# Kernel optimization log

Measured on AMD Instinct MI355X. Metric: run time of the kernel, lower is better.

Reference implementation:

```python
import jax, jax.numpy as jnp
import numpy as np

N, E, F, H = 50000, 800000, 128, 8
D = F // H
SCALING = D ** (-0.5)


def setup_inputs() -> dict:
    key = jax.random.key(0)
    ks = jax.random.split(key, 10)
    w_scale = (2.0 / (F + F)) ** 0.5  # approx xavier
    return {
        "feat": jax.random.normal(ks[0], (N, F), jnp.float32),
        "edge_feat": jax.random.normal(ks[1], (E, F), jnp.float32),
        "Wq": jax.random.normal(ks[2], (F, F), jnp.float32) * w_scale,
        "Wk": jax.random.normal(ks[3], (F, F), jnp.float32) * w_scale,
        "Wv": jax.random.normal(ks[4], (F, F), jnp.float32) * w_scale,
        "Wnode": jax.random.normal(ks[5], (F, F), jnp.float32) * w_scale,
        "Wedge": jax.random.normal(ks[6], (H, F), jnp.float32) * w_scale,
        "Wgate": jax.random.normal(ks[7], (H, F), jnp.float32) * w_scale,
        "src": jax.random.randint(ks[8], (E,), 0, N, jnp.int32),
        "dst": jax.random.randint(ks[9], (E,), 0, N, jnp.int32),
    }


def reference(feat, edge_feat, Wq, Wk, Wv, Wnode, Wedge, Wgate, src, dst):
    # dense projections: [N, F] -> [N, H, D]
    q = (feat @ Wq.T).reshape(N, H, D)
    k = (feat @ Wk.T).reshape(N, H, D)
    v = (feat @ Wv.T).reshape(N, H, D)

    # u_dot_v: per-edge, per-head dot product q[src] . k[dst]  -> [E, H]
    a = jnp.einsum("ehd,ehd->eh", q[src], k[dst])

    # edge bias and sigmoid gates from edge features (use_efeats=True)
    e_bias = edge_feat @ Wedge.T            # [E, H]
    gates = jax.nn.sigmoid(edge_feat @ Wgate.T)  # [E, H]

    # clamp, add bias, divide by scaling (i.e. multiply by sqrt(D), as in source)
    logits = (jnp.clip(a, -5.0, 5.0) + e_bias) / SCALING  # [E, H]

    # edge softmax: segmented (per-destination-node) softmax over incoming edges
    m = jax.ops.segment_max(logits, dst, num_segments=N)  # [N, H]
    ex = jnp.exp(logits - m[dst])                          # [E, H]
    s = jax.ops.segment_sum(ex, dst, num_segments=N)       # [N, H]
    sa = (ex / s[dst]) * gates                             # [E, H]

    # weighted scatter-aggregation: sum_e v[src_e] * sa_e grouped by dst
    agg = jax.ops.segment_sum(v[src] * sa[:, :, None], dst, num_segments=N)  # [N, H, D]

    rst = agg.reshape(N, F) @ Wnode.T  # [N, F]
    return rst
```

## Files before the change

kernel.cpp:

```cpp
#include <hip/hip_runtime.h>
#include <hip/hip_fp16.h>
#include <math.h>

#define NN 50000
#define NE 800000
#define FF 128
#define QKV_BLOCKS 782
#define EDGE_GEMM_BLOCKS 12500
#define AGG_BLOCKS 12500
#define HIST_BLOCKS 3125

using short8 = __attribute__((ext_vector_type(8))) short;
using f32x4  = __attribute__((ext_vector_type(4))) float;
using h2     = __attribute__((ext_vector_type(2))) _Float16;

#define EXP_SCALE 5.770780163555851f

__device__ __forceinline__ short f2bf(float x){
  union { float f; unsigned u; } c; c.f = x;
  unsigned r = c.u + 0x7FFFu + ((c.u >> 16) & 1u);
  return (short)(r >> 16);
}
__device__ __forceinline__ float bf2f(short h){
  union { unsigned u; float f; } c; c.u = ((unsigned)(unsigned short)h) << 16;
  return c.f;
}
__device__ __forceinline__ float hdot2(h2 a, h2 b){
#if __has_builtin(__builtin_amdgcn_fdot2)
  return __builtin_amdgcn_fdot2(a, b, 0.f, false);
#else
  return (float)a[0]*(float)b[0] + (float)a[1]*(float)b[1];
#endif
}
__device__ __forceinline__ float fexp2(float x){
#if __has_builtin(__builtin_amdgcn_exp2f)
  return __builtin_amdgcn_exp2f(x);
#else
  return exp2f(x);
#endif
}
__device__ __forceinline__ float clamp5(float x){
#if __has_builtin(__builtin_amdgcn_fmed3f)
  return __builtin_amdgcn_fmed3f(x, -5.f, 5.f);
#else
  return fminf(fmaxf(x, -5.f), 5.f);
#endif
}

#define PREP_A_FRAGS(arow)                                              \
  short8 ahi[4], alo[4];                                                \
  {                                                                     \
    _Pragma("unroll")                                                   \
    for (int kk = 0; kk < 4; kk++){                                     \
      float4 lo4 = *(const float4*)((arow) + kk*32);                    \
      float4 hi4 = *(const float4*)((arow) + kk*32 + 4);                \
      float xs[8] = {lo4.x, lo4.y, lo4.z, lo4.w, hi4.x, hi4.y, hi4.z, hi4.w}; \
      short8 th, tl;                                                    \
      _Pragma("unroll")                                                 \
      for (int j = 0; j < 8; j++){                                      \
        short hh = f2bf(xs[j]);                                         \
        th[j] = hh;                                                     \
        tl[j] = f2bf(xs[j] - bf2f(hh));                                 \
      }                                                                 \
      ahi[kk] = th; alo[kk] = tl;                                       \
    }                                                                   \
  }

#define GEMM_CT_3CHAIN(bh, bl, accout)                                  \
  f32x4 accout;                                                         \
  {                                                                     \
    f32x4 a1 = {0.f,0.f,0.f,0.f}, a2 = {0.f,0.f,0.f,0.f}, a3 = {0.f,0.f,0.f,0.f}; \
    _Pragma("unroll")                                                   \
    for (int kk = 0; kk < 4; kk++){                                     \
      short8 bfh = *(const short8*)((bh) + kk*32);                      \
      short8 bfl = *(const short8*)((bl) + kk*32);                      \
      a1 = __builtin_amdgcn_mfma_f32_16x16x32_bf16(ahi[kk], bfh, a1, 0, 0, 0); \
      a2 = __builtin_amdgcn_mfma_f32_16x16x32_bf16(ahi[kk], bfl, a2, 0, 0, 0); \
      a3 = __builtin_amdgcn_mfma_f32_16x16x32_bf16(alo[kk], bfh, a3, 0, 0, 0); \
    }                                                                   \
    accout = a1 + a2 + a3;                                              \
  }

__global__ void k_cvt_w(const float* __restrict__ Wq, const float* __restrict__ Wk,
                        const float* __restrict__ Wv, const float* __restrict__ Wn,
                        const float* __restrict__ We, const float* __restrict__ Wg,
                        short* bqkv, short* bn, short* bc, int* __restrict__ deg){
  int i = blockIdx.x*256 + threadIdx.x;
  if (i < NN) deg[i] = 0;
  if (i < 16384){
    const float* W[3] = {Wq, Wk, Wv};
    #pragma unroll
    for (int j = 0; j < 3; j++){
      float x = W[j][i];
      short hi = f2bf(x);
      bqkv[j*16384 + i] = hi;
      bqkv[49152 + j*16384 + i] = f2bf(x - bf2f(hi));
    }
    float xn = Wn[i];
    short hn = f2bf(xn);
    bn[i] = hn; bn[i + 16384] = f2bf(xn - bf2f(hn));
  }
  if (i < 2048){
    float x = (i < 1024) ? We[i] : Wg[i-1024];
    short hi = f2bf(x);
    bc[i] = hi; bc[i + 2048] = f2bf(x - bf2f(hi));
  }
}

__global__ void k_qkv_hist(const float* __restrict__ A, const short* __restrict__ B,
                           _Float16* __restrict__ C,
                           const int* __restrict__ dst, int* __restrict__ deg){
  if (blockIdx.x >= QKV_BLOCKS){
    int e = (blockIdx.x - QKV_BLOCKS)*256 + threadIdx.x;
    if (e < NE) atomicAdd(&deg[dst[e]], 1);
    return;
  }
  const int NC = 384;
  int w = threadIdx.x >> 6, lane = threadIdx.x & 63;
  int row0 = (blockIdx.x*4 + w)*16;
  if (row0 >= NN) return;
  int r  = lane & 15;
  int kq = lane >> 4;

  const short* Bhi = B;
  const short* Blo = B + (size_t)NC*FF;

  const float* arow = A + (size_t)(row0 + r)*FF + kq*8;
  PREP_A_FRAGS(arow)

  for (int ct = 0; ct < (NC >> 4); ct++){
    const short* bh = Bhi + (size_t)(ct*16 + r)*FF + kq*8;
    const short* bl = Blo + (size_t)(ct*16 + r)*FF + kq*8;
    GEMM_CT_3CHAIN(bh, bl, acc)
    _Float16* crow = C + (size_t)(row0 + kq*4)*NC + ct*16 + r;
    #pragma unroll
    for (int i = 0; i < 4; i++) crow[(size_t)i*NC] = (_Float16)acc[i];
  }
}

__global__ void k_scan(const int* __restrict__ deg, int* __restrict__ rowptr,
                       int* __restrict__ cursor){
  __shared__ int sums[1024];
  const int CH = 52;
  int t = threadIdx.x;
  int base = t*CH;
  int vals[CH];
  int s = 0;
  #pragma unroll
  for (int i = 0; i < 13; i++){
    int idx = base + i*4;
    int4 v;
    if (idx + 3 < NN) v = *(const int4*)(deg + idx);
    else v = make_int4(idx < NN ? deg[idx] : 0, idx+1 < NN ? deg[idx+1] : 0,
                       idx+2 < NN ? deg[idx+2] : 0, idx+3 < NN ? deg[idx+3] : 0);
    vals[i*4+0]=v.x; vals[i*4+1]=v.y; vals[i*4+2]=v.z; vals[i*4+3]=v.w;
    s += v.x + v.y + v.z + v.w;
  }
  sums[t] = s; __syncthreads();
  for (int off = 1; off < 1024; off <<= 1){
    int val = (t >= off) ? sums[t-off] : 0;
    __syncthreads();
    sums[t] += val;
    __syncthreads();
  }
  int run = sums[t] - s;
  #pragma unroll
  for (int i = 0; i < 13; i++){
    int idx = base + i*4;
    int4 w0;
    w0.x = run; run += vals[i*4+0];
    w0.y = run; run += vals[i*4+1];
    w0.z = run; run += vals[i*4+2];
    w0.w = run; run += vals[i*4+3];
    if (idx + 3 < NN){
      *(int4*)(rowptr + idx) = w0;
      *(int4*)(cursor + idx) = w0;
    } else {
      if (idx   < NN){ rowptr[idx  ] = w0.x; cursor[idx  ] = w0.x; }
      if (idx+1 < NN){ rowptr[idx+1] = w0.y; cursor[idx+1] = w0.y; }
      if (idx+2 < NN){ rowptr[idx+2] = w0.z; cursor[idx+2] = w0.z; }
      if (idx+3 < NN){ rowptr[idx+3] = w0.w; cursor[idx+3] = w0.w; }
    }
  }
}

__global__ void k_edge(const float* __restrict__ A, const short* __restrict__ B,
                       const int* __restrict__ src, const int* __restrict__ dst,
                       int* __restrict__ cursor, int2* __restrict__ list,
                       float* __restrict__ ebg2){
  int w = threadIdx.x >> 6, lane = threadIdx.x & 63;
  int row0 = (blockIdx.x*4 + w)*16;
  int r  = lane & 15;
  int kq = lane >> 4;

  if (kq == 0){
    int e = row0 + r;
    int d = dst[e];
    int s = src[e];
    int pos = atomicAdd(&cursor[d], 1);
    list[pos] = make_int2(s, e);
  }

  const float* arow = A + (size_t)(row0 + r)*FF + kq*8;
  PREP_A_FRAGS(arow)

  const short* bh = B + (size_t)r*FF + kq*8;
  const short* bl = bh + 2048;
  GEMM_CT_3CHAIN(bh, bl, acc)

  #pragma unroll
  for (int i = 0; i < 4; i++){
    int e = row0 + kq*4 + i;
    float x = acc[i];
    float outv; int col;
    if (r < 8){ outv = x*EXP_SCALE; col = r*2; }
    else      { outv = 1.f/(1.f + __expf(-x)); col = (r-8)*2 + 1; }
    ebg2[(size_t)e*16 + col] = outv;
  }
}

__global__ void k_aggregate(const _Float16* __restrict__ qkv, const float* __restrict__ ebg2,
                            const int* __restrict__ rowptr, const int* __restrict__ cursor,
                            const int2* __restrict__ list, float* __restrict__ agg){
  int w = threadIdx.x >> 6, lane = threadIdx.x & 63;
  int node = blockIdx.x*4 + w;
  if (node >= NN) return;
  int beg = rowptr[node], end = cursor[node];
  h2 kk = *(const h2*)&qkv[(size_t)node*384 + 128 + lane*2];
  int h = lane >> 3;
  float ssA=0.f, a0A=0.f, a1A=0.f;
  float ssB=0.f, a0B=0.f, a1B=0.f;
  for (int i0 = beg; i0 < end; i0 += 64){
    int nb = min(end - i0, 64);
    int2 es = (i0 + lane < end) ? list[i0 + lane] : make_int2(0,0);
    int j = 0;
    for (; j + 1 < nb; j += 2){
      int sA = __shfl(es.x, j);
      int eA = __shfl(es.y, j);
      int sB = __shfl(es.x, j+1);
      int eB = __shfl(es.y, j+1);
      const _Float16* rA = qkv + (size_t)sA*384 + lane*2;
      const _Float16* rB = qkv + (size_t)sB*384 + lane*2;
      h2 qA = *(const h2*)rA;
      h2 vA = *(const h2*)(rA + 256);
      h2 qB = *(const h2*)rB;
      h2 vB = *(const h2*)(rB + 256);
      float2 ebA = *(const float2*)&ebg2[(size_t)eA*16 + h*2];
      float2 ebB = *(const float2*)&ebg2[(size_t)eB*16 + h*2];
      float pA = hdot2(qA, kk);
      float pB = hdot2(qB, kk);
      pA += __shfl_xor(pA, 1); pB += __shfl_xor(pB, 1);
      pA += __shfl_xor(pA, 2); pB += __shfl_xor(pB, 2);
      pA += __shfl_xor(pA, 4); pB += __shfl_xor(pB, 4);
      float tA = fexp2(fmaf(clamp5(pA), EXP_SCALE, ebA.x));
      float tB = fexp2(fmaf(clamp5(pB), EXP_SCALE, ebB.x));
      float wA = tA * ebA.y;
      float wB = tB * ebB.y;
      a0A += wA*(float)vA[0]; a1A += wA*(float)vA[1]; ssA += tA;
      a0B += wB*(float)vB[0]; a1B += wB*(float)vB[1]; ssB += tB;
    }
    if (j < nb){
      int sA = __shfl(es.x, j);
      int eA = __shfl(es.y, j);
      const _Float16* rA = qkv + (size_t)sA*384 + lane*2;
      h2 qA = *(const h2*)rA;
      h2 vA = *(const h2*)(rA + 256);
      float2 ebA = *(const float2*)&ebg2[(size_t)eA*16 + h*2];
      float pA = hdot2(qA, kk);
      pA += __shfl_xor(pA, 1); pA += __shfl_xor(pA, 2); pA += __shfl_xor(pA, 4);
      float tA = fexp2(fmaf(clamp5(pA), EXP_SCALE, ebA.x));
      float wA = tA * ebA.y;
      a0A += wA*(float)vA[0]; a1A += wA*(float)vA[1]; ssA += tA;
    }
  }
  float ss = ssA + ssB;
  float inv = (end > beg) ? 1.f/ss : 0.f;
  *(float2*)&agg[(size_t)node*FF + lane*2] = make_float2((a0A+a0B)*inv, (a1A+a1B)*inv);
}

__global__ void k_gemm_out(const float* __restrict__ A, const short* __restrict__ B,
                           float* __restrict__ C){
  const int NC = 128;
  int w = threadIdx.x >> 6, lane = threadIdx.x & 63;
  int row0 = (blockIdx.x*4 + w)*16;
  if (row0 >= NN) return;
  int r  = lane & 15;
  int kq = lane >> 4;

  const short* Bhi = B;
  const short* Blo = B + (size_t)NC*FF;

  const float* arow = A + (size_t)(row0 + r)*FF + kq*8;
  PREP_A_FRAGS(arow)

  for (int ct = 0; ct < (NC >> 4); ct++){
    const short* bh = Bhi + (size_t)(ct*16 + r)*FF + kq*8;
    const short* bl = Blo + (size_t)(ct*16 + r)*FF + kq*8;
    GEMM_CT_3CHAIN(bh, bl, acc)
    float* crow = C + (size_t)(row0 + kq*4)*NC + ct*16 + r;
    #pragma unroll
    for (int i = 0; i < 4; i++) crow[(size_t)i*NC] = acc[i];
  }
}

extern "C" void kernel_launch(void* const* d_in, const int* in_sizes, int n_in,
                              void* d_out, int out_size, void* d_ws, size_t ws_size,
                              hipStream_t stream) {
  const float* feat      = (const float*)d_in[0];
  const float* edge_feat = (const float*)d_in[1];
  const float* Wq        = (const float*)d_in[2];
  const float* Wk        = (const float*)d_in[3];
  const float* Wv        = (const float*)d_in[4];
  const float* Wnode     = (const float*)d_in[5];
  const float* Wedge     = (const float*)d_in[6];
  const float* Wgate     = (const float*)d_in[7];
  const int*   src       = (const int*)d_in[8];
  const int*   dst       = (const int*)d_in[9];
  float* out = (float*)d_out;

  char* p = (char*)d_ws;
  auto alloc = [&](size_t bytes)->char*{
    char* r = p; p += (bytes + 255) & ~(size_t)255; return r;
  };
  _Float16* qkv = (_Float16*)alloc((size_t)NN*384*2);
  float* ebg2   = (float*)alloc((size_t)NE*16*4);
  float* agg    = (float*)alloc((size_t)NN*FF*4);
  int*   deg    = (int*)  alloc((size_t)NN*4);
  int*   rowptr = (int*)  alloc((size_t)NN*4);
  int*   cursor = (int*)  alloc((size_t)NN*4);
  int2*  list   = (int2*) alloc((size_t)NE*8);
  short* bqkv   = (short*)alloc(2*49152*2);
  short* bn     = (short*)alloc(2*16384*2);
  short* bc     = (short*)alloc(2*2048*2);

  k_cvt_w<<<196, 256, 0, stream>>>(Wq, Wk, Wv, Wnode, Wedge, Wgate, bqkv, bn, bc, deg);

  k_qkv_hist<<<QKV_BLOCKS + HIST_BLOCKS, 256, 0, stream>>>(feat, bqkv, qkv, dst, deg);

  k_scan<<<1, 1024, 0, stream>>>(deg, rowptr, cursor);

  k_edge<<<EDGE_GEMM_BLOCKS, 256, 0, stream>>>(edge_feat, bc, src, dst, cursor, list, ebg2);

  k_aggregate<<<AGG_BLOCKS, 256, 0, stream>>>(qkv, ebg2, rowptr, cursor, list, agg);

  k_gemm_out<<<QKV_BLOCKS, 256, 0, stream>>>(agg, bn, out);
}
```

Baseline: 359.9 us.

## Interleave QKV GEMM into edge kernel, store edge bias/gate as fp16, nontemporal loads

Moves the node QKV projection out of the histogram kernel and interleaves its blocks, one in every 17, with the edge-feature GEMM blocks so both streaming workloads share one launch. The per-edge bias and gate buffer is stored as fp16 instead of fp32, halving its write and gather traffic; the scale is applied in the aggregate kernel instead. Nontemporal loads are used for streamed edge features, the edge list and the bias/gate gathers to reduce cache pollution. The fp16 bias storage adds rounding error to the logits before exponentiation.

```diff
diff --git a/kernel.cpp b/kernel.cpp
--- a/kernel.cpp
+++ b/kernel.cpp
@@ -7,12 +7,15 @@
 #define FF 128
 #define QKV_BLOCKS 782
 #define EDGE_GEMM_BLOCKS 12500
+#define MERGED_BLOCKS 13282
 #define AGG_BLOCKS 12500
 #define HIST_BLOCKS 3125
 
 using short8 = __attribute__((ext_vector_type(8))) short;
 using f32x4  = __attribute__((ext_vector_type(4))) float;
+using fv4    = __attribute__((ext_vector_type(4))) float;
 using h2     = __attribute__((ext_vector_type(2))) _Float16;
+using i32x2  = __attribute__((ext_vector_type(2))) int;
 
 #define EXP_SCALE 5.770780163555851f
 
@@ -47,14 +50,20 @@
 #endif
 }
 
-#define PREP_A_FRAGS(arow)                                              \
+#define PREP_A_FRAGS_NT(arow, NT)                                       \
   short8 ahi[4], alo[4];                                                \
   {                                                                     \
     _Pragma("unroll")                                                   \
     for (int kk = 0; kk < 4; kk++){                                     \
-      float4 lo4 = *(const float4*)((arow) + kk*32);                    \
-      float4 hi4 = *(const float4*)((arow) + kk*32 + 4);                \
-      float xs[8] = {lo4.x, lo4.y, lo4.z, lo4.w, hi4.x, hi4.y, hi4.z, hi4.w}; \
+      fv4 lo4, hi4;                                                     \
+      if (NT){                                                          \
+        lo4 = __builtin_nontemporal_load((const fv4*)((arow) + kk*32)); \
+        hi4 = __builtin_nontemporal_load((const fv4*)((arow) + kk*32 + 4)); \
+      } else {                                                          \
+        lo4 = *(const fv4*)((arow) + kk*32);                            \
+        hi4 = *(const fv4*)((arow) + kk*32 + 4);                        \
+      }                                                                 \
+      float xs[8] = {lo4[0], lo4[1], lo4[2], lo4[3], hi4[0], hi4[1], hi4[2], hi4[3]}; \
       short8 th, tl;                                                    \
       _Pragma("unroll")                                                 \
       for (int j = 0; j < 8; j++){                                      \
@@ -69,16 +78,16 @@
 #define GEMM_CT_3CHAIN(bh, bl, accout)                                  \
   f32x4 accout;                                                         \
   {                                                                     \
-    f32x4 a1 = {0.f,0.f,0.f,0.f}, a2 = {0.f,0.f,0.f,0.f}, a3 = {0.f,0.f,0.f,0.f}; \
+    f32x4 c1 = {0.f,0.f,0.f,0.f}, c2 = {0.f,0.f,0.f,0.f}, c3 = {0.f,0.f,0.f,0.f}; \
     _Pragma("unroll")                                                   \
     for (int kk = 0; kk < 4; kk++){                                     \
       short8 bfh = *(const short8*)((bh) + kk*32);                      \
       short8 bfl = *(const short8*)((bl) + kk*32);                      \
-      a1 = __builtin_amdgcn_mfma_f32_16x16x32_bf16(ahi[kk], bfh, a1, 0, 0, 0); \
-      a2 = __builtin_amdgcn_mfma_f32_16x16x32_bf16(ahi[kk], bfl, a2, 0, 0, 0); \
-      a3 = __builtin_amdgcn_mfma_f32_16x16x32_bf16(alo[kk], bfh, a3, 0, 0, 0); \
+      c1 = __builtin_amdgcn_mfma_f32_16x16x32_bf16(ahi[kk], bfh, c1, 0, 0, 0); \
+      c2 = __builtin_amdgcn_mfma_f32_16x16x32_bf16(ahi[kk], bfl, c2, 0, 0, 0); \
+      c3 = __builtin_amdgcn_mfma_f32_16x16x32_bf16(alo[kk], bfh, c3, 0, 0, 0); \
     }                                                                   \
-    accout = a1 + a2 + a3;                                              \
+    accout = c1 + c2 + c3;                                              \
   }
 
 __global__ void k_cvt_w(const float* __restrict__ Wq, const float* __restrict__ Wk,
@@ -107,35 +116,9 @@
   }
 }
 
-__global__ void k_qkv_hist(const float* __restrict__ A, const short* __restrict__ B,
-                           _Float16* __restrict__ C,
-                           const int* __restrict__ dst, int* __restrict__ deg){
-  if (blockIdx.x >= QKV_BLOCKS){
-    int e = (blockIdx.x - QKV_BLOCKS)*256 + threadIdx.x;
-    if (e < NE) atomicAdd(&deg[dst[e]], 1);
-    return;
-  }
-  const int NC = 384;
-  int w = threadIdx.x >> 6, lane = threadIdx.x & 63;
-  int row0 = (blockIdx.x*4 + w)*16;
-  if (row0 >= NN) return;
-  int r  = lane & 15;
-  int kq = lane >> 4;
-
-  const short* Bhi = B;
-  const short* Blo = B + (size_t)NC*FF;
-
-  const float* arow = A + (size_t)(row0 + r)*FF + kq*8;
-  PREP_A_FRAGS(arow)
-
-  for (int ct = 0; ct < (NC >> 4); ct++){
-    const short* bh = Bhi + (size_t)(ct*16 + r)*FF + kq*8;
-    const short* bl = Blo + (size_t)(ct*16 + r)*FF + kq*8;
-    GEMM_CT_3CHAIN(bh, bl, acc)
-    _Float16* crow = C + (size_t)(row0 + kq*4)*NC + ct*16 + r;
-    #pragma unroll
-    for (int i = 0; i < 4; i++) crow[(size_t)i*NC] = (_Float16)acc[i];
-  }
+__global__ void k_hist(const int* __restrict__ dst, int* __restrict__ deg){
+  int e = blockIdx.x*256 + threadIdx.x;
+  if (e < NE) atomicAdd(&deg[dst[e]], 1);
 }
 
 __global__ void k_scan(const int* __restrict__ deg, int* __restrict__ rowptr,
@@ -184,14 +167,39 @@
   }
 }
 
-__global__ void k_edge(const float* __restrict__ A, const short* __restrict__ B,
-                       const int* __restrict__ src, const int* __restrict__ dst,
-                       int* __restrict__ cursor, int2* __restrict__ list,
-                       float* __restrict__ ebg2){
+__global__ void k_edge_qkv(const float* __restrict__ EF, const short* __restrict__ Bc,
+                           const int* __restrict__ src, const int* __restrict__ dst,
+                           int* __restrict__ cursor, int2* __restrict__ list,
+                           _Float16* __restrict__ ebg,
+                           const float* __restrict__ A, const short* __restrict__ Bqkv,
+                           _Float16* __restrict__ C){
+  int bid = blockIdx.x;
   int w = threadIdx.x >> 6, lane = threadIdx.x & 63;
-  int row0 = (blockIdx.x*4 + w)*16;
   int r  = lane & 15;
   int kq = lane >> 4;
+
+  if (bid % 17 == 0){
+    const int NC = 384;
+    int qb = bid / 17;
+    int row0 = (qb*4 + w)*16;
+    if (row0 >= NN) return;
+    const short* Bhi = Bqkv;
+    const short* Blo = Bqkv + (size_t)NC*FF;
+    const float* arow = A + (size_t)(row0 + r)*FF + kq*8;
+    PREP_A_FRAGS_NT(arow, 1)
+    for (int ct = 0; ct < (NC >> 4); ct++){
+      const short* bh = Bhi + (size_t)(ct*16 + r)*FF + kq*8;
+      const short* bl = Blo + (size_t)(ct*16 + r)*FF + kq*8;
+      GEMM_CT_3CHAIN(bh, bl, acc)
+      _Float16* crow = C + (size_t)(row0 + kq*4)*NC + ct*16 + r;
+      #pragma unroll
+      for (int i = 0; i < 4; i++) crow[(size_t)i*NC] = (_Float16)acc[i];
+    }
+    return;
+  }
+
+  int eb = bid - (bid/17 + 1);
+  int row0 = (eb*4 + w)*16;
 
   if (kq == 0){
     int e = row0 + r;
@@ -201,10 +209,10 @@
     list[pos] = make_int2(s, e);
   }
 
-  const float* arow = A + (size_t)(row0 + r)*FF + kq*8;
-  PREP_A_FRAGS(arow)
-
-  const short* bh = B + (size_t)r*FF + kq*8;
+  const float* arow = EF + (size_t)(row0 + r)*FF + kq*8;
+  PREP_A_FRAGS_NT(arow, 1)
+
+  const short* bh = Bc + (size_t)r*FF + kq*8;
   const short* bl = bh + 2048;
   GEMM_CT_3CHAIN(bh, bl, acc)
 
@@ -212,14 +220,14 @@
   for (int i = 0; i < 4; i++){
     int e = row0 + kq*4 + i;
     float x = acc[i];
-    float outv; int col;
-    if (r < 8){ outv = x*EXP_SCALE; col = r*2; }
-    else      { outv = 1.f/(1.f + __expf(-x)); col = (r-8)*2 + 1; }
-    ebg2[(size_t)e*16 + col] = outv;
-  }
-}
-
-__global__ void k_aggregate(const _Float16* __restrict__ qkv, const float* __restrict__ ebg2,
+    _Float16 outv; int col;
+    if (r < 8){ outv = (_Float16)x; col = r*2; }
+    else      { outv = (_Float16)(1.f/(1.f + __expf(-x))); col = (r-8)*2 + 1; }
+    ebg[(size_t)e*16 + col] = outv;
+  }
+}
+
+__global__ void k_aggregate(const _Float16* __restrict__ qkv, const _Float16* __restrict__ ebg,
                             const int* __restrict__ rowptr, const int* __restrict__ cursor,
                             const int2* __restrict__ list, float* __restrict__ agg){
   int w = threadIdx.x >> 6, lane = threadIdx.x & 63;
@@ -232,44 +240,48 @@
   float ssB=0.f, a0B=0.f, a1B=0.f;
   for (int i0 = beg; i0 < end; i0 += 64){
     int nb = min(end - i0, 64);
-    int2 es = (i0 + lane < end) ? list[i0 + lane] : make_int2(0,0);
+    i32x2 es = {0, 0};
+    if (i0 + lane < end) es = __builtin_nontemporal_load((const i32x2*)(list + i0 + lane));
     int j = 0;
     for (; j + 1 < nb; j += 2){
-      int sA = __shfl(es.x, j);
-      int eA = __shfl(es.y, j);
-      int sB = __shfl(es.x, j+1);
-      int eB = __shfl(es.y, j+1);
+      int sA = __shfl(es[0], j);
+      int eA = __shfl(es[1], j);
+      int sB = __shfl(es[0], j+1);
+      int eB = __shfl(es[1], j+1);
       const _Float16* rA = qkv + (size_t)sA*384 + lane*2;
       const _Float16* rB = qkv + (size_t)sB*384 + lane*2;
       h2 qA = *(const h2*)rA;
       h2 vA = *(const h2*)(rA + 256);
       h2 qB = *(const h2*)rB;
       h2 vB = *(const h2*)(rB + 256);
-      float2 ebA = *(const float2*)&ebg2[(size_t)eA*16 + h*2];
-      float2 ebB = *(const float2*)&ebg2[(size_t)eB*16 + h*2];
+      unsigned ubA = __builtin_nontemporal_load((const unsigned*)(ebg + (size_t)eA*16 + h*2));
+      unsigned ubB = __builtin_nontemporal_load((const unsigned*)(ebg + (size_t)eB*16 + h*2));
+      h2 bgA = *(h2*)&ubA;
+      h2 bgB = *(h2*)&ubB;
       float pA = hdot2(qA, kk);
       float pB = hdot2(qB, kk);
       pA += __shfl_xor(pA, 1); pB += __shfl_xor(pB, 1);
       pA += __shfl_xor(pA, 2); pB += __shfl_xor(pB, 2);
       pA += __shfl_xor(pA, 4); pB += __shfl_xor(pB, 4);
-      float tA = fexp2(fmaf(clamp5(pA), EXP_SCALE, ebA.x));
-      float tB = fexp2(fmaf(clamp5(pB), EXP_SCALE, ebB.x));
-      float wA = tA * ebA.y;
-      float wB = tB * ebB.y;
+      float tA = fexp2((clamp5(pA) + (float)bgA[0]) * EXP_SCALE);
+      float tB = fexp2((clamp5(pB) + (float)bgB[0]) * EXP_SCALE);
+      float wA = tA * (float)bgA[1];
+      float wB = tB * (float)bgB[1];
       a0A += wA*(float)vA[0]; a1A += wA*(float)vA[1]; ssA += tA;
       a0B += wB*(float)vB[0]; a1B += wB*(float)vB[1]; ssB += tB;
     }
     if (j < nb){
-      int sA = __shfl(es.x, j);
-      int eA = __shfl(es.y, j);
+      int sA = __shfl(es[0], j);
+      int eA = __shfl(es[1], j);
       const _Float16* rA = qkv + (size_t)sA*384 + lane*2;
       h2 qA = *(const h2*)rA;
       h2 vA = *(const h2*)(rA + 256);
-      float2 ebA = *(const float2*)&ebg2[(size_t)eA*16 + h*2];
+      unsigned ubA = __builtin_nontemporal_load((const unsigned*)(ebg + (size_t)eA*16 + h*2));
+      h2 bgA = *(h2*)&ubA;
       float pA = hdot2(qA, kk);
       pA += __shfl_xor(pA, 1); pA += __shfl_xor(pA, 2); pA += __shfl_xor(pA, 4);
-      float tA = fexp2(fmaf(clamp5(pA), EXP_SCALE, ebA.x));
-      float wA = tA * ebA.y;
+      float tA = fexp2((clamp5(pA) + (float)bgA[0]) * EXP_SCALE);
+      float wA = tA * (float)bgA[1];
       a0A += wA*(float)vA[0]; a1A += wA*(float)vA[1]; ssA += tA;
     }
   }
@@ -291,7 +303,7 @@
   const short* Blo = B + (size_t)NC*FF;
 
   const float* arow = A + (size_t)(row0 + r)*FF + kq*8;
-  PREP_A_FRAGS(arow)
+  PREP_A_FRAGS_NT(arow, 0)
 
   for (int ct = 0; ct < (NC >> 4); ct++){
     const short* bh = Bhi + (size_t)(ct*16 + r)*FF + kq*8;
@@ -323,7 +335,7 @@
     char* r = p; p += (bytes + 255) & ~(size_t)255; return r;
   };
   _Float16* qkv = (_Float16*)alloc((size_t)NN*384*2);
-  float* ebg2   = (float*)alloc((size_t)NE*16*4);
+  _Float16* ebg = (_Float16*)alloc((size_t)NE*16*2);
   float* agg    = (float*)alloc((size_t)NN*FF*4);
   int*   deg    = (int*)  alloc((size_t)NN*4);
   int*   rowptr = (int*)  alloc((size_t)NN*4);
@@ -335,13 +347,14 @@
 
   k_cvt_w<<<196, 256, 0, stream>>>(Wq, Wk, Wv, Wnode, Wedge, Wgate, bqkv, bn, bc, deg);
 
-  k_qkv_hist<<<QKV_BLOCKS + HIST_BLOCKS, 256, 0, stream>>>(feat, bqkv, qkv, dst, deg);
+  k_hist<<<HIST_BLOCKS, 256, 0, stream>>>(dst, deg);
 
   k_scan<<<1, 1024, 0, stream>>>(deg, rowptr, cursor);
 
-  k_edge<<<EDGE_GEMM_BLOCKS, 256, 0, stream>>>(edge_feat, bc, src, dst, cursor, list, ebg2);
-
-  k_aggregate<<<AGG_BLOCKS, 256, 0, stream>>>(qkv, ebg2, rowptr, cursor, list, agg);
+  k_edge_qkv<<<MERGED_BLOCKS, 256, 0, stream>>>(edge_feat, bc, src, dst, cursor, list, ebg,
+                                                feat, bqkv, qkv);
+
+  k_aggregate<<<AGG_BLOCKS, 256, 0, stream>>>(qkv, ebg, rowptr, cursor, list, agg);
 
   k_gemm_out<<<QKV_BLOCKS, 256, 0, stream>>>(agg, bn, out);
 }
```

Result: slower. 410.4 us (+14.0%).
